# Kernel optimization log

Hardware: AMD Instinct MI355X
Metric: run time of the kernel (lower is better)

## Reference

```python
import jax, jax.numpy as jnp
import numpy as np

N = 50000      # nodes
E = 800000     # edges (before self-loops)
IN = 256       # input_dim
HID = 72       # hidden_dim
HEADS = 4
NEG_SLOPE = 0.2  # PyG GATConv default leaky-relu slope


def setup_inputs() -> dict:
    key = jax.random.key(0)
    ks = jax.random.split(key, 16)
    rn = lambda k, shape: jax.random.normal(k, shape, jnp.float32) * 0.05
    return {
        "x": jax.random.normal(ks[0], (N, IN), jnp.float32),
        "edge_index": jax.random.randint(ks[1], (2, E), 0, N),
        "W_in": rn(ks[2], (IN, HID)), "b_in": jnp.zeros((HID,), jnp.float32),
        "W1": rn(ks[3], (HID, HEADS * HID)),
        "a_src1": rn(ks[4], (HEADS, HID)), "a_dst1": rn(ks[5], (HEADS, HID)),
        "b1": jnp.zeros((HEADS * HID,), jnp.float32),
        "W2": rn(ks[6], (HEADS * HID, HID)),
        "a_src2": rn(ks[7], (1, HID)), "a_dst2": rn(ks[8], (1, HID)),
        "b2": jnp.zeros((HID,), jnp.float32),
        "W3": rn(ks[9], (HID, HID)),
        "a_src3": rn(ks[10], (1, HID)), "a_dst3": rn(ks[11], (1, HID)),
        "b3": jnp.zeros((HID,), jnp.float32),
        "Ws1": rn(ks[12], (HID, 32)), "bs1": jnp.zeros((32,), jnp.float32),
        "Ws2": rn(ks[13], (32, 1)), "bs2": jnp.zeros((1,), jnp.float32),
    }


def gat_conv(x, src, dst, W, a_src, a_dst, bias, concat):
    # PyG GATConv (eval mode): per-head linear, leaky-relu attention logits,
    # segment softmax over incoming edges per destination, scatter-aggregate.
    H, C = a_src.shape
    h = (x @ W).reshape(-1, H, C)                      # [N, H, C]
    logit_s = jnp.einsum('nhc,hc->nh', h, a_src)       # [N, H]
    logit_d = jnp.einsum('nhc,hc->nh', h, a_dst)       # [N, H]
    e = jax.nn.leaky_relu(logit_s[src] + logit_d[dst], NEG_SLOPE)   # [Et, H]
    emax = jax.ops.segment_max(e, dst, num_segments=N)
    emax = jnp.where(jnp.isfinite(emax), emax, 0.0)
    p = jnp.exp(e - emax[dst])
    denom = jax.ops.segment_sum(p, dst, num_segments=N)
    alpha = p / jnp.maximum(denom[dst], 1e-16)         # [Et, H]
    out = jax.ops.segment_sum(h[src] * alpha[:, :, None], dst, num_segments=N)
    out = out.reshape(-1, H * C) if concat else out.mean(axis=1)
    return out + bias


def reference(x, edge_index, W_in, b_in,
              W1, a_src1, a_dst1, b1,
              W2, a_src2, a_dst2, b2,
              W3, a_src3, a_dst3, b3,
              Ws1, bs1, Ws2, bs2):
    loops = jnp.arange(N)                              # PyG add_self_loops=True
    src = jnp.concatenate([edge_index[0], loops])
    dst = jnp.concatenate([edge_index[1], loops])
    x0 = x @ W_in + b_in                               # [N, HID]
    h = jax.nn.elu(gat_conv(x0, src, dst, W1, a_src1, a_dst1, b1, True))
    h = jax.nn.elu(gat_conv(h, src, dst, W2, a_src2, a_dst2, b2, False))
    h = jax.nn.elu(gat_conv(h, src, dst, W3, a_src3, a_dst3, b3, False))
    h = h + x0
    score = jax.nn.relu(h @ Ws1 + bs1) @ Ws2 + bs2     # dropout = identity (eval)
    return score.squeeze(-1)                           # [N]
```

## Files before the change

### kernel.cpp

```cpp
#include <hip/hip_runtime.h>
#include <hip/hip_fp16.h>
#include <cmath>

#define NN 50000
#define EE 800000
#define ET (EE + NN)
#define IN_DIM 256
#define HID 72
#define CAP 96

typedef __attribute__((ext_vector_type(8))) short s8v;
typedef __attribute__((ext_vector_type(4))) short s4v;
typedef __attribute__((ext_vector_type(4))) float f4v;
typedef __attribute__((ext_vector_type(2))) float f2v;

__device__ __forceinline__ ushort f2bf(float x) {
    uint u = __float_as_uint(x);
    return (ushort)((u + 0x7fffu + ((u >> 16) & 1u)) >> 16);
}
__device__ __forceinline__ float bf2f(ushort h) {
    return __uint_as_float(((uint)h) << 16);
}
__device__ __forceinline__ void split4(const float4& v, s4v& h, s4v& l) {
    ushort h0 = f2bf(v.x), h1 = f2bf(v.y), h2 = f2bf(v.z), h3 = f2bf(v.w);
    h = (s4v){(short)h0, (short)h1, (short)h2, (short)h3};
    l = (s4v){(short)f2bf(v.x - bf2f(h0)), (short)f2bf(v.y - bf2f(h1)),
              (short)f2bf(v.z - bf2f(h2)), (short)f2bf(v.w - bf2f(h3))};
}
__device__ __forceinline__ f4v mfma16(s8v a, s8v b, f4v c) {
    return __builtin_amdgcn_mfma_f32_16x16x32_bf16(a, b, c, 0, 0, 0);
}
__device__ __forceinline__ f2v unpack_h2(uint pv) {
    __half2 hv = __builtin_bit_cast(__half2, pv);
    return (f2v){__low2float(hv), __high2float(hv)};
}
__device__ __forceinline__ uint pack_h2(float a, float b) {
    __half2 hp = __floats2half2_rn(a, b);
    return __builtin_bit_cast(uint, hp);
}
__device__ __forceinline__ f2v fma2(float w, f2v c, f2v a) {
    return __builtin_elementwise_fma((f2v){w, w}, c, a);
}

__device__ __forceinline__ void wsplit_one(const float* W, int ldw, int K,
        int idx, short* outH, short* outL) {
    int h = idx / (72 * K);
    int rem = idx - h * 72 * K;
    int n = rem / K, k = rem - n * K;
    float v = W[(size_t)k * ldw + h * 72 + n];
    ushort hi = f2bf(v);
    outH[idx] = (short)hi;
    outL[idx] = (short)f2bf(v - bf2f(hi));
}

#define PR0 18432
#define PR1 (PR0 + 20736)
#define PR2 (PR1 + 20736)
#define PR3 (PR2 + 5184)
#define PR4 (PR3 + 288)
#define PRTOT (PR4 + NN)

__global__ __launch_bounds__(256) void prep_kernel(
        const float* __restrict__ W_in, const float* __restrict__ W1,
        const float* __restrict__ W2, const float* __restrict__ W3,
        const float* __restrict__ a_src, const float* __restrict__ a_dst,
        short* __restrict__ BtInH, short* __restrict__ BtInL,
        short* __restrict__ Bt1H, short* __restrict__ Bt1L,
        short* __restrict__ Bt2H, short* __restrict__ Bt2L,
        short* __restrict__ Bt3H, short* __restrict__ Bt3L,
        float* __restrict__ wsrc, float* __restrict__ wdst,
        int* __restrict__ deg, ushort* __restrict__ ell) {
    int gid = blockIdx.x * 256 + threadIdx.x;
    if (gid < PR0) {
        wsplit_one(W_in, 72, 256, gid, BtInH, BtInL);
    } else if (gid < PR1) {
        wsplit_one(W1, 288, 72, gid - PR0, Bt1H, Bt1L);
    } else if (gid < PR2) {
        wsplit_one(W2, 72, 288, gid - PR1, Bt2H, Bt2L);
    } else if (gid < PR3) {
        wsplit_one(W3, 72, 72, gid - PR2, Bt3H, Bt3L);
    } else if (gid < PR4) {
        int j = gid - PR3;
        int h = j / HID, k = j % HID;
        const float* wrow = W1 + (size_t)k * (4 * HID) + h * HID;
        const float* as = a_src + h * HID;
        const float* ad = a_dst + h * HID;
        float s = 0.f, d = 0.f;
        for (int c = 0; c < HID; ++c) {
            float w = wrow[c];
            s = fmaf(w, as[c], s);
            d = fmaf(w, ad[c], d);
        }
        wsrc[j] = s;
        wdst[j] = d;
    } else if (gid < PRTOT) {
        int i = gid - PR4;
        deg[i] = 1;
        ell[(size_t)i * CAP] = (ushort)i;
    }
}

template <int NLOGIT, bool ELU_EPI, bool BATCHED, bool PACKOUT, bool APACK, bool ADJ>
__global__ __launch_bounds__(256) void gemm_mfma(
        const void* __restrict__ Ain, const short* __restrict__ BtH,
        const short* __restrict__ BtL, const float* __restrict__ bias,
        float* __restrict__ C, uint* __restrict__ Cp, int ldp,
        const float* __restrict__ lvs, const float* __restrict__ lvd,
        float* __restrict__ ls, float* __restrict__ ld,
        int M, int K, int lda, int Nfull,
        const int* __restrict__ eiw, int* __restrict__ degw,
        ushort* __restrict__ ellw, int gemmBlocks) {
    __shared__ __align__(16) short AhS[64 * 40], AlS[64 * 40];
    __shared__ __align__(16) short BhS[80 * 40], BlS[80 * 40];

    int tid = threadIdx.x;

    if (ADJ && (int)blockIdx.x >= gemmBlocks) {
        int t = (blockIdx.x - gemmBlocks) * 256 + tid;
        int i0 = t * 4;
        if (i0 < EE) {
            int4 s4 = *(const int4*)(eiw + i0);
            int4 d4 = *(const int4*)(eiw + EE + i0);
            int ss[4] = {s4.x, s4.y, s4.z, s4.w};
            int dd[4] = {d4.x, d4.y, d4.z, d4.w};
            #pragma unroll
            for (int u = 0; u < 4; ++u) {
                int pos = atomicAdd(&degw[dd[u]], 1);
                if (pos < CAP) ellw[(size_t)dd[u] * CAP + pos] = (ushort)ss[u];
            }
        }
        return;
    }

    int row0 = blockIdx.x * 64;
    int hh = BATCHED ? blockIdx.y : 0;
    int aoff = BATCHED ? hh * (APACK ? 36 : 72) : 0;
    int coff = BATCHED ? hh * 72 : 0;
    const short* bhg = BtH + (size_t)hh * 72 * K;
    const short* blg = BtL + (size_t)hh * 72 * K;

    for (int i = tid; i < 8 * 40; i += 256) {
        BhS[72 * 40 + i] = 0;
        BlS[72 * 40 + i] = 0;
    }

    int w = tid >> 6;
    int lane = tid & 63;
    int q = lane >> 4, l16 = lane & 15;

    f4v acc[5];
    #pragma unroll
    for (int f = 0; f < 5; ++f) acc[f] = (f4v)0.f;

    int ar = tid >> 2;
    int aseg = tid & 3;
    bool arok = (row0 + ar) < M;
    const float* aptrf = nullptr;
    const uint*  aptru = nullptr;
    if constexpr (APACK) {
        aptru = (const uint*)Ain + (size_t)(row0 + ar) * lda + aoff;
    } else {
        aptrf = (const float*)Ain + (size_t)(row0 + ar) * lda + aoff;
    }
    int bn0 = tid >> 2, bq0 = tid & 3;
    int bn1 = (tid + 256) >> 2;

    float4 va, vb;
    s8v bh0, bl0, bh1, bl1;
    auto gload = [&](int k0) {
        va = (float4){0, 0, 0, 0};
        vb = (float4){0, 0, 0, 0};
        int ka = k0 + aseg * 8;
        if constexpr (APACK) {
            if (arok && ka < K) {
                uint4 u = *(const uint4*)(aptru + (ka >> 1));
                f2v p0 = unpack_h2(u.x), p1 = unpack_h2(u.y);
                f2v p2 = unpack_h2(u.z), p3 = unpack_h2(u.w);
                va = (float4){p0.x, p0.y, p1.x, p1.y};
                vb = (float4){p2.x, p2.y, p3.x, p3.y};
            }
        } else {
            if (arok && ka < K)     va = *(const float4*)(aptrf + ka);
            if (arok && ka + 4 < K) vb = *(const float4*)(aptrf + ka + 4);
        }
        bh0 = (s8v)0; bl0 = (s8v)0;
        int kb = k0 + bq0 * 8;
        if (kb < K) {
            bh0 = *(const s8v*)(bhg + (size_t)bn0 * K + kb);
            bl0 = *(const s8v*)(blg + (size_t)bn0 * K + kb);
        }
        bh1 = (s8v)0; bl1 = (s8v)0;
        if (tid < 32 && kb < K) {
            bh1 = *(const s8v*)(bhg + (size_t)bn1 * K + kb);
            bl1 = *(const s8v*)(blg + (size_t)bn1 * K + kb);
        }
    };
    auto commit = [&]() {
        s4v h0, l0, h1, l1;
        split4(va, h0, l0);
        split4(vb, h1, l1);
        *(s4v*)&AhS[ar * 40 + aseg * 8]     = h0;
        *(s4v*)&AhS[ar * 40 + aseg * 8 + 4] = h1;
        *(s4v*)&AlS[ar * 40 + aseg * 8]     = l0;
        *(s4v*)&AlS[ar * 40 + aseg * 8 + 4] = l1;
        *(s8v*)&BhS[bn0 * 40 + bq0 * 8] = bh0;
        *(s8v*)&BlS[bn0 * 40 + bq0 * 8] = bl0;
        if (tid < 32) {
            *(s8v*)&BhS[bn1 * 40 + bq0 * 8] = bh1;
            *(s8v*)&BlS[bn1 * 40 + bq0 * 8] = bl1;
        }
    };

    int ntiles = (K + 31) / 32;
    gload(0);
    for (int t = 0; t < ntiles; ++t) {
        commit();
        __syncthreads();
        if (t + 1 < ntiles) gload((t + 1) * 32);
        s8v ah = *(const s8v*)&AhS[(w * 16 + l16) * 40 + q * 8];
        s8v al = *(const s8v*)&AlS[(w * 16 + l16) * 40 + q * 8];
        #pragma unroll
        for (int f = 0; f < 5; ++f) {
            s8v bh = *(const s8v*)&BhS[(f * 16 + l16) * 40 + q * 8];
            s8v bl = *(const s8v*)&BlS[(f * 16 + l16) * 40 + q * 8];
            acc[f] = mfma16(ah, bh, acc[f]);
            acc[f] = mfma16(ah, bl, acc[f]);
            acc[f] = mfma16(al, bh, acc[f]);
        }
        __syncthreads();
    }

    float v[5][4];
    #pragma unroll
    for (int f = 0; f < 5; ++f) {
        int col = f * 16 + l16;
        bool cv = col < 72;
        #pragma unroll
        for (int r = 0; r < 4; ++r) {
            float t = acc[f][r];
            if (cv && bias) t += bias[coff + col];
            if (ELU_EPI) t = (t > 0.f) ? t : expm1f(t);
            v[f][r] = cv ? t : 0.f;
        }
    }
    if (NLOGIT > 0) {
        #pragma unroll
        for (int h2 = 0; h2 < NLOGIT; ++h2) {
            #pragma unroll
            for (int r = 0; r < 4; ++r) {
                float s = 0.f, d = 0.f;
                #pragma unroll
                for (int f = 0; f < 5; ++f) {
                    int col = f * 16 + l16;
                    float lw = (col < 72) ? lvs[h2 * 72 + col] : 0.f;
                    float dw = (col < 72) ? lvd[h2 * 72 + col] : 0.f;
                    s = fmaf(v[f][r], lw, s);
                    d = fmaf(v[f][r], dw, d);
                }
                s += __shfl_xor(s, 1); s += __shfl_xor(s, 2);
                s += __shfl_xor(s, 4); s += __shfl_xor(s, 8);
                d += __shfl_xor(d, 1); d += __shfl_xor(d, 2);
                d += __shfl_xor(d, 4); d += __shfl_xor(d, 8);
                int gr = row0 + w * 16 + q * 4 + r;
                if (l16 == 0 && gr < M) {
                    ls[gr * NLOGIT + h2] = s;
                    ld[gr * NLOGIT + h2] = d;
                }
            }
        }
    }
    if (PACKOUT) {
        #pragma unroll
        for (int f = 0; f < 5; ++f) {
            int col = f * 16 + l16;
            #pragma unroll
            for (int r = 0; r < 4; ++r) {
                float vo = __shfl_xor(v[f][r], 1);
                if ((l16 & 1) == 0 && col < 72) {
                    int gr = row0 + w * 16 + q * 4 + r;
                    if (gr < M) {
                        Cp[(size_t)gr * ldp + ((coff + col) >> 1)] =
                            pack_h2(v[f][r], vo);
                    }
                }
            }
        }
    }
    if (C != nullptr) {
        #pragma unroll
        for (int f = 0; f < 5; ++f) {
            int col = f * 16 + l16;
            if (col >= 72) continue;
            #pragma unroll
            for (int r = 0; r < 4; ++r) {
                int gr = row0 + w * 16 + q * 4 + r;
                if (gr < M) C[(size_t)gr * Nfull + coff + col] = v[f][r];
            }
        }
    }
}

template <int H, bool EPI, bool ADD_RES, bool POUT, bool SCORE>
__global__ __launch_bounds__(64) void agg_gather(
        const uint* __restrict__ featp,
        const float* __restrict__ ls, const float* __restrict__ ld,
        const int* __restrict__ degv, const ushort* __restrict__ ell,
        const float* __restrict__ bias, const float* __restrict__ res,
        float* __restrict__ out, uint* __restrict__ outp,
        const float* __restrict__ Ws1, const float* __restrict__ bs1,
        const float* __restrict__ Ws2, const float* __restrict__ bs2,
        int n) {
    __shared__ float wsh[64 * H];
    __shared__ int ssh[64];
    __shared__ float srow[HID];
    int wid = blockIdx.x;
    int lane = threadIdx.x;
    int deg = min(degv[wid], CAP);
    const ushort* row = ell + (size_t)wid * CAP;

    float ldh[H];
    if (H == 4) {
        float4 t = ((const float4*)ld)[wid];
        ldh[0] = t.x; ldh[1] = t.y; ldh[2] = t.z; ldh[3] = t.w;
    } else {
        ldh[0] = ld[wid];
    }

    f2v acc2[H];
    #pragma unroll
    for (int h = 0; h < H; ++h) acc2[h] = (f2v)0.f;

    if (deg <= 64) {
        bool act = lane < deg;
        int s = row[act ? lane : 0];
        ssh[lane] = s;
        float e[H];
        float ev[H];
        if (H == 4) {
            float4 lv = ((const float4*)ls)[s];
            ev[0] = lv.x; ev[1] = lv.y; ev[2] = lv.z; ev[3] = lv.w;
        } else {
            ev[0] = ls[s];
        }
        #pragma unroll
        for (int h = 0; h < H; ++h) {
            float vv = ev[h] + ldh[h];
            vv = (vv > 0.f) ? vv : 0.2f * vv;
            e[h] = act ? vv : -__builtin_inff();
        }
        float wv[H];
        #pragma unroll
        for (int h = 0; h < H; ++h) {
            float mh = e[h];
            #pragma unroll
            for (int off = 32; off; off >>= 1) mh = fmaxf(mh, __shfl_xor(mh, off));
            float ph = act ? expf(e[h] - mh) : 0.f;
            float sh = ph;
            #pragma unroll
            for (int off = 32; off; off >>= 1) sh += __shfl_xor(sh, off);
            wv[h] = ph / fmaxf(sh, 1e-16f);
        }
        if (H == 4) {
            ((float4*)wsh)[lane] = (float4){wv[0], wv[1], wv[2], wv[3]};
        } else {
            wsh[lane] = wv[0];
        }
        __syncthreads();

        int nb = (deg + 7) & ~7;
        const uint* rowbase = featp + (lane < 36 ? lane : 0);
        for (int t = 0; t < nb; t += 8) {
            int si[8];
            #pragma unroll
            for (int u = 0; u < 8; ++u) si[u] = ssh[t + u];
            uint pv[8];
            #pragma unroll
            for (int u = 0; u < 8; ++u) pv[u] = rowbase[(size_t)si[u] * 36];
            #pragma unroll
            for (int u = 0; u < 8; ++u) {
                f2v c2 = unpack_h2(pv[u]);
                if constexpr (H == 4) {
                    float4 we = ((const float4*)wsh)[t + u];
                    acc2[0] = fma2(we.x, c2, acc2[0]);
                    acc2[1] = fma2(we.y, c2, acc2[1]);
                    acc2[2] = fma2(we.z, c2, acc2[2]);
                    acc2[3] = fma2(we.w, c2, acc2[3]);
                } else {
                    acc2[0] = fma2(wsh[t + u], c2, acc2[0]);
                }
            }
        }
    } else {
        float m[H];
        #pragma unroll
        for (int h = 0; h < H; ++h) m[h] = -__builtin_inff();
        for (int i = lane; i < deg; i += 64) {
            int s = row[i];
            float e[H];
            if (H == 4) {
                float4 lv = ((const float4*)ls)[s];
                e[0] = lv.x; e[1] = lv.y; e[2] = lv.z; e[3] = lv.w;
            } else {
                e[0] = ls[s];
            }
            #pragma unroll
            for (int h = 0; h < H; ++h) {
                float vv = e[h] + ldh[h];
                vv = (vv > 0.f) ? vv : 0.2f * vv;
                m[h] = fmaxf(m[h], vv);
            }
        }
        #pragma unroll
        for (int h = 0; h < H; ++h)
            #pragma unroll
            for (int off = 32; off; off >>= 1) m[h] = fmaxf(m[h], __shfl_xor(m[h], off));

        float ssum[H];
        #pragma unroll
        for (int h = 0; h < H; ++h) ssum[h] = 0.f;
        for (int i = lane; i < deg; i += 64) {
            int s = row[i];
            float e[H];
            if (H == 4) {
                float4 lv = ((const float4*)ls)[s];
                e[0] = lv.x; e[1] = lv.y; e[2] = lv.z; e[3] = lv.w;
            } else {
                e[0] = ls[s];
            }
            #pragma unroll
            for (int h = 0; h < H; ++h) {
                float vv = e[h] + ldh[h];
                vv = (vv > 0.f) ? vv : 0.2f * vv;
                ssum[h] += expf(vv - m[h]);
            }
        }
        #pragma unroll
        for (int h = 0; h < H; ++h)
            #pragma unroll
            for (int off = 32; off; off >>= 1) ssum[h] += __shfl_xor(ssum[h], off);
        float inv[H];
        #pragma unroll
        for (int h = 0; h < H; ++h) inv[h] = 1.f / fmaxf(ssum[h], 1e-16f);

        for (int base = 0; base < deg; base += 64) {
            int i = base + lane;
            int lim = min(64, deg - base);
            if (i < deg) {
                int s = row[i];
                ssh[lane] = s;
                float e[H];
                if (H == 4) {
                    float4 lv = ((const float4*)ls)[s];
                    e[0] = lv.x; e[1] = lv.y; e[2] = lv.z; e[3] = lv.w;
                } else {
                    e[0] = ls[s];
                }
                if (H == 4) {
                    float p0 = expf(((e[0] + ldh[0] > 0.f) ? e[0] + ldh[0] : 0.2f * (e[0] + ldh[0])) - m[0]) * inv[0];
                    float p1 = expf(((e[1] + ldh[1] > 0.f) ? e[1] + ldh[1] : 0.2f * (e[1] + ldh[1])) - m[1]) * inv[1];
                    float p2 = expf(((e[2] + ldh[2] > 0.f) ? e[2] + ldh[2] : 0.2f * (e[2] + ldh[2])) - m[2]) * inv[2];
                    float p3 = expf(((e[3] + ldh[3] > 0.f) ? e[3] + ldh[3] : 0.2f * (e[3] + ldh[3])) - m[3]) * inv[3];
                    ((float4*)wsh)[lane] = (float4){p0, p1, p2, p3};
                } else {
                    float vv = e[0] + ldh[0];
                    vv = (vv > 0.f) ? vv : 0.2f * vv;
                    wsh[lane] = expf(vv - m[0]) * inv[0];
                }
            }
            __syncthreads();
            for (int t = 0; t < lim; ++t) {
                uint pv = featp[(size_t)ssh[t] * 36 + (lane < 36 ? lane : 0)];
                f2v c2 = unpack_h2(pv);
                if constexpr (H == 4) {
                    float4 we = ((const float4*)wsh)[t];
                    acc2[0] = fma2(we.x, c2, acc2[0]);
                    acc2[1] = fma2(we.y, c2, acc2[1]);
                    acc2[2] = fma2(we.z, c2, acc2[2]);
                    acc2[3] = fma2(we.w, c2, acc2[3]);
                } else {
                    acc2[0] = fma2(wsh[t], c2, acc2[0]);
                }
            }
            __syncthreads();
        }
    }

    if (lane < 36) {
        #pragma unroll
        for (int h = 0; h < H; ++h) {
            float v0 = acc2[h].x, v1 = acc2[h].y;
            if (EPI) {
                v0 += bias[2 * lane];
                v1 += bias[2 * lane + 1];
                v0 = (v0 > 0.f) ? v0 : expm1f(v0);
                v1 = (v1 > 0.f) ? v1 : expm1f(v1);
                if (ADD_RES) {
                    float2 rr = *(const float2*)&res[(size_t)wid * HID + 2 * lane];
                    v0 += rr.x; v1 += rr.y;
                }
            }
            if (POUT) {
                outp[(size_t)wid * (H * 36) + h * 36 + lane] = pack_h2(v0, v1);
            } else if (SCORE) {
                srow[2 * lane] = v0;
                srow[2 * lane + 1] = v1;
            } else {
                *(float2*)&out[(size_t)wid * (H * HID) + h * HID + 2 * lane] =
                    (float2){v0, v1};
            }
        }
    }
    if (SCORE) {
        __syncthreads();
        if (lane < 32) {
            float acc = bs1[lane];
            #pragma unroll 8
            for (int c = 0; c < HID; ++c)
                acc = fmaf(srow[c], Ws1[c * 32 + lane], acc);
            float v = fmaxf(acc, 0.f) * Ws2[lane];
            #pragma unroll
            for (int off = 16; off; off >>= 1) v += __shfl_down(v, off, 32);
            if (lane == 0) out[wid] = v + bs2[0];
        }
    }
}

extern "C" void kernel_launch(void* const* d_in, const int* in_sizes, int n_in,
                              void* d_out, int out_size, void* d_ws, size_t ws_size,
                              hipStream_t stream) {
    const float* x      = (const float*)d_in[0];
    const int*   ei     = (const int*)  d_in[1];
    const float* W_in   = (const float*)d_in[2];
    const float* b_in   = (const float*)d_in[3];
    const float* W1     = (const float*)d_in[4];
    const float* a_src1 = (const float*)d_in[5];
    const float* a_dst1 = (const float*)d_in[6];
    const float* b1     = (const float*)d_in[7];
    const float* W2     = (const float*)d_in[8];
    const float* a_src2 = (const float*)d_in[9];
    const float* a_dst2 = (const float*)d_in[10];
    const float* b2     = (const float*)d_in[11];
    const float* W3     = (const float*)d_in[12];
    const float* a_src3 = (const float*)d_in[13];
    const float* a_dst3 = (const float*)d_in[14];
    const float* b3     = (const float*)d_in[15];
    const float* Ws1    = (const float*)d_in[16];
    const float* bs1    = (const float*)d_in[17];
    const float* Ws2    = (const float*)d_in[18];
    const float* bs2    = (const float*)d_in[19];
    float* out = (float*)d_out;

    float* ws    = (float*)d_ws;
    float* x0    = ws;
    float* ls    = x0 + (size_t)NN * HID;
    float* ld    = ls + (size_t)NN * 4;
    float* wsrc1 = ld + (size_t)NN * 4;
    float* wdst1 = wsrc1 + 288;
    int* deg     = (int*)(wdst1 + 288);
    ushort* ell  = (ushort*)(deg + NN);
    uintptr_t bp = ((uintptr_t)(ell + (size_t)NN * CAP) + 15) & ~(uintptr_t)15;
    short* BtInH = (short*)bp;
    short* BtInL = BtInH + 18432;
    short* Bt1H  = BtInL + 18432;
    short* Bt1L  = Bt1H + 20736;
    short* Bt2H  = Bt1L + 20736;
    short* Bt2L  = Bt2H + 20736;
    short* Bt3H  = Bt2L + 20736;
    short* Bt3L  = Bt3H + 5184;
    uint*  x0p   = (uint*)(Bt3L + 5184);
    uint*  a1p   = x0p + (size_t)NN * 36;
    uint*  h1p   = a1p + (size_t)NN * 144;
    uint*  hp2p  = h1p + (size_t)NN * 144;
    uint*  h2p   = hp2p + (size_t)NN * 36;
    uint*  hp3p  = h2p + (size_t)NN * 36;

    prep_kernel<<<(PRTOT + 255) / 256, 256, 0, stream>>>(
        W_in, W1, W2, W3, a_src1, a_dst1,
        BtInH, BtInL, Bt1H, Bt1L, Bt2H, Bt2L, Bt3H, Bt3L, wsrc1, wdst1,
        deg, ell);

    const int mblocks = (NN + 63) / 64;
    const int adjBlocks = (EE / 4 + 255) / 256;
    gemm_mfma<4, false, false, true, false, true>
        <<<dim3(mblocks + adjBlocks, 1), 256, 0, stream>>>(
        x, BtInH, BtInL, b_in, x0, x0p, 36, wsrc1, wdst1, ls, ld,
        NN, IN_DIM, IN_DIM, HID, ei, deg, ell, mblocks);
    agg_gather<4, false, false, true, false><<<NN, 64, 0, stream>>>(
        x0p, ls, ld, deg, ell, nullptr, nullptr, nullptr, a1p,
        nullptr, nullptr, nullptr, nullptr, NN);
    gemm_mfma<0, true, true, true, true, false><<<dim3(mblocks, 4), 256, 0, stream>>>(
        a1p, Bt1H, Bt1L, b1, nullptr, h1p, 144, nullptr, nullptr, nullptr, nullptr,
        NN, HID, 144, 0, nullptr, nullptr, nullptr, 0);
    gemm_mfma<1, false, false, true, true, false><<<dim3(mblocks, 1), 256, 0, stream>>>(
        h1p, Bt2H, Bt2L, nullptr, nullptr, hp2p, 36, a_src2, a_dst2, ls, ld,
        NN, 288, 144, 0, nullptr, nullptr, nullptr, 0);
    agg_gather<1, true, false, true, false><<<NN, 64, 0, stream>>>(
        hp2p, ls, ld, deg, ell, b2, nullptr, nullptr, h2p,
        nullptr, nullptr, nullptr, nullptr, NN);
    gemm_mfma<1, false, false, true, true, false><<<dim3(mblocks, 1), 256, 0, stream>>>(
        h2p, Bt3H, Bt3L, nullptr, nullptr, hp3p, 36, a_src3, a_dst3, ls, ld,
        NN, HID, 36, 0, nullptr, nullptr, nullptr, 0);
    agg_gather<1, true, true, false, true><<<NN, 64, 0, stream>>>(
        hp3p, ls, ld, deg, ell, b3, x0, out, nullptr,
        Ws1, bs1, Ws2, bs2, NN);
}
```

Measured before the change: 366.2 us.

## Fuse edge aggregation with following per-node GEMM into one agg_gemm kernel

Adds an agg_gemm kernel in which each 256-thread block gathers and softmax-aggregates 64 destination nodes into shared memory as fp16. It then runs the next layer's split-bf16 MFMA GEMM directly from that tile, with optional bias/ELU and attention-logit epilogues. It replaces the layer-1 agg+GEMM pair and the layer-2 agg + layer-3 GEMM pair, removing intermediate a1p/h2p global round-trips and two launches. Layer-3 logits go to separate ls3/ld3 buffers so ls/ld, which are still being read by other blocks, are not overwritten. The trade-off is lower parallelism during the gather phase: each wave now processes 16 nodes serially instead of one node per 64-thread block.

```diff
diff --git a/kernel.cpp b/kernel.cpp
--- a/kernel.cpp
+++ b/kernel.cpp
@@ -40,6 +40,17 @@
 }
 __device__ __forceinline__ f2v fma2(float w, f2v c, f2v a) {
     return __builtin_elementwise_fma((f2v){w, w}, c, a);
+}
+__device__ __forceinline__ void unpack_split8(uint4 u, s8v& ah, s8v& al) {
+    f2v p0 = unpack_h2(u.x), p1 = unpack_h2(u.y);
+    f2v p2 = unpack_h2(u.z), p3 = unpack_h2(u.w);
+    float x[8] = {p0.x, p0.y, p1.x, p1.y, p2.x, p2.y, p3.x, p3.y};
+    #pragma unroll
+    for (int i = 0; i < 8; ++i) {
+        ushort hi = f2bf(x[i]);
+        ah[i] = (short)hi;
+        al[i] = (short)f2bf(x[i] - bf2f(hi));
+    }
 }
 
 __device__ __forceinline__ void wsplit_one(const float* W, int ldw, int K,
@@ -300,6 +311,271 @@
     }
 }
 
+template <int H, int NH, bool AGG_EPI, int NLOGIT, bool GELU>
+__global__ __launch_bounds__(256) void agg_gemm(
+        const uint* __restrict__ featp,
+        const float* __restrict__ ls, const float* __restrict__ ld,
+        const int* __restrict__ degv, const ushort* __restrict__ ell,
+        const float* __restrict__ abias,
+        const short* __restrict__ BtH, const short* __restrict__ BtL,
+        const float* __restrict__ gbias,
+        const float* __restrict__ lvs, const float* __restrict__ lvd,
+        float* __restrict__ lso, float* __restrict__ ldo,
+        uint* __restrict__ outp, int ldp) {
+    __shared__ __align__(16) uint aS[64][H * 36 + 4];
+    int tid = threadIdx.x;
+    int w = tid >> 6;
+    int lane = tid & 63;
+    int row0 = blockIdx.x * 64;
+
+    for (int i = 0; i < 16; ++i) {
+        int nl = w * 16 + i;
+        int n = row0 + nl;
+        if (n >= NN) {
+            if (lane < 36) {
+                #pragma unroll
+                for (int h = 0; h < H; ++h) aS[nl][h * 36 + lane] = 0u;
+            }
+            continue;
+        }
+        int deg = min(degv[n], CAP);
+        const ushort* row = ell + (size_t)n * CAP;
+        float ldh[H];
+        if (H == 4) {
+            float4 t = ((const float4*)ld)[n];
+            ldh[0] = t.x; ldh[1] = t.y; ldh[2] = t.z; ldh[3] = t.w;
+        } else {
+            ldh[0] = ld[n];
+        }
+        f2v acc2[H];
+        #pragma unroll
+        for (int h = 0; h < H; ++h) acc2[h] = (f2v)0.f;
+        const uint* rowbase = featp + (lane < 36 ? lane : 0);
+
+        if (deg <= 64) {
+            bool act = lane < deg;
+            int s = row[act ? lane : 0];
+            float ev[H];
+            if (H == 4) {
+                float4 lv = ((const float4*)ls)[s];
+                ev[0] = lv.x; ev[1] = lv.y; ev[2] = lv.z; ev[3] = lv.w;
+            } else {
+                ev[0] = ls[s];
+            }
+            float wv[H];
+            #pragma unroll
+            for (int h = 0; h < H; ++h) {
+                float vv = ev[h] + ldh[h];
+                vv = (vv > 0.f) ? vv : 0.2f * vv;
+                float e = act ? vv : -__builtin_inff();
+                float mh = e;
+                #pragma unroll
+                for (int off = 32; off; off >>= 1) mh = fmaxf(mh, __shfl_xor(mh, off));
+                float ph = act ? expf(e - mh) : 0.f;
+                float sh = ph;
+                #pragma unroll
+                for (int off = 32; off; off >>= 1) sh += __shfl_xor(sh, off);
+                wv[h] = ph / fmaxf(sh, 1e-16f);
+            }
+            int nb = (deg + 7) & ~7;
+            for (int t = 0; t < nb; t += 8) {
+                int si[8];
+                #pragma unroll
+                for (int u = 0; u < 8; ++u) si[u] = __shfl(s, t + u);
+                uint pv[8];
+                #pragma unroll
+                for (int u = 0; u < 8; ++u) pv[u] = rowbase[(size_t)si[u] * 36];
+                #pragma unroll
+                for (int u = 0; u < 8; ++u) {
+                    f2v c2 = unpack_h2(pv[u]);
+                    #pragma unroll
+                    for (int h = 0; h < H; ++h) {
+                        float wu = __shfl(wv[h], t + u);
+                        acc2[h] = fma2(wu, c2, acc2[h]);
+                    }
+                }
+            }
+        } else {
+            float m[H];
+            #pragma unroll
+            for (int h = 0; h < H; ++h) m[h] = -__builtin_inff();
+            for (int i2 = lane; i2 < deg; i2 += 64) {
+                int s = row[i2];
+                float ev[H];
+                if (H == 4) {
+                    float4 lv = ((const float4*)ls)[s];
+                    ev[0] = lv.x; ev[1] = lv.y; ev[2] = lv.z; ev[3] = lv.w;
+                } else {
+                    ev[0] = ls[s];
+                }
+                #pragma unroll
+                for (int h = 0; h < H; ++h) {
+                    float vv = ev[h] + ldh[h];
+                    vv = (vv > 0.f) ? vv : 0.2f * vv;
+                    m[h] = fmaxf(m[h], vv);
+                }
+            }
+            #pragma unroll
+            for (int h = 0; h < H; ++h)
+                #pragma unroll
+                for (int off = 32; off; off >>= 1) m[h] = fmaxf(m[h], __shfl_xor(m[h], off));
+            float ssum[H];
+            #pragma unroll
+            for (int h = 0; h < H; ++h) ssum[h] = 0.f;
+            for (int i2 = lane; i2 < deg; i2 += 64) {
+                int s = row[i2];
+                float ev[H];
+                if (H == 4) {
+                    float4 lv = ((const float4*)ls)[s];
+                    ev[0] = lv.x; ev[1] = lv.y; ev[2] = lv.z; ev[3] = lv.w;
+                } else {
+                    ev[0] = ls[s];
+                }
+                #pragma unroll
+                for (int h = 0; h < H; ++h) {
+                    float vv = ev[h] + ldh[h];
+                    vv = (vv > 0.f) ? vv : 0.2f * vv;
+                    ssum[h] += expf(vv - m[h]);
+                }
+            }
+            #pragma unroll
+            for (int h = 0; h < H; ++h)
+                #pragma unroll
+                for (int off = 32; off; off >>= 1) ssum[h] += __shfl_xor(ssum[h], off);
+            float inv[H];
+            #pragma unroll
+            for (int h = 0; h < H; ++h) inv[h] = 1.f / fmaxf(ssum[h], 1e-16f);
+            for (int base = 0; base < deg; base += 64) {
+                int i2 = base + lane;
+                int lim = min(64, deg - base);
+                int s = row[(i2 < deg) ? i2 : base];
+                float pw[H];
+                float ev[H];
+                if (H == 4) {
+                    float4 lv = ((const float4*)ls)[s];
+                    ev[0] = lv.x; ev[1] = lv.y; ev[2] = lv.z; ev[3] = lv.w;
+                } else {
+                    ev[0] = ls[s];
+                }
+                #pragma unroll
+                for (int h = 0; h < H; ++h) {
+                    float vv = ev[h] + ldh[h];
+                    vv = (vv > 0.f) ? vv : 0.2f * vv;
+                    pw[h] = (i2 < deg) ? expf(vv - m[h]) * inv[h] : 0.f;
+                }
+                for (int t = 0; t < lim; ++t) {
+                    int sv = __shfl(s, t);
+                    uint pv = rowbase[(size_t)sv * 36];
+                    f2v c2 = unpack_h2(pv);
+                    #pragma unroll
+                    for (int h = 0; h < H; ++h) {
+                        float wu = __shfl(pw[h], t);
+                        acc2[h] = fma2(wu, c2, acc2[h]);
+                    }
+                }
+            }
+        }
+
+        if (lane < 36) {
+            #pragma unroll
+            for (int h = 0; h < H; ++h) {
+                float v0 = acc2[h].x, v1 = acc2[h].y;
+                if (AGG_EPI) {
+                    v0 += abias[2 * lane];
+                    v1 += abias[2 * lane + 1];
+                    v0 = (v0 > 0.f) ? v0 : expm1f(v0);
+                    v1 = (v1 > 0.f) ? v1 : expm1f(v1);
+                }
+                aS[nl][h * 36 + lane] = pack_h2(v0, v1);
+            }
+        }
+    }
+    __syncthreads();
+
+    int q = lane >> 4, l16 = lane & 15;
+    int arow = w * 16 + l16;
+    for (int h = 0; h < NH; ++h) {
+        f4v acc[5];
+        #pragma unroll
+        for (int f = 0; f < 5; ++f) acc[f] = (f4v)0.f;
+        #pragma unroll
+        for (int t3 = 0; t3 < 3; ++t3) {
+            int ks = t3 * 32 + q * 8;
+            s8v ah = (s8v)0, al = (s8v)0;
+            if (ks < 72) {
+                uint4 u = *(const uint4*)&aS[arow][h * 36 + (ks >> 1)];
+                unpack_split8(u, ah, al);
+            }
+            #pragma unroll
+            for (int f = 0; f < 5; ++f) {
+                int bn = f * 16 + l16;
+                s8v bh = (s8v)0, bl = (s8v)0;
+                if (bn < 72 && ks < 72) {
+                    bh = *(const s8v*)(BtH + ((size_t)h * 72 + bn) * 72 + ks);
+                    bl = *(const s8v*)(BtL + ((size_t)h * 72 + bn) * 72 + ks);
+                }
+                acc[f] = mfma16(ah, bh, acc[f]);
+                acc[f] = mfma16(ah, bl, acc[f]);
+                acc[f] = mfma16(al, bh, acc[f]);
+            }
+        }
+        float v[5][4];
+        #pragma unroll
+        for (int f = 0; f < 5; ++f) {
+            int col = f * 16 + l16;
+            bool cv = col < 72;
+            #pragma unroll
+            for (int r = 0; r < 4; ++r) {
+                float t = acc[f][r];
+                if (cv && gbias) t += gbias[h * 72 + col];
+                if (GELU) t = (t > 0.f) ? t : expm1f(t);
+                v[f][r] = cv ? t : 0.f;
+            }
+        }
+        if (NLOGIT > 0) {
+            #pragma unroll
+            for (int h2 = 0; h2 < NLOGIT; ++h2) {
+                #pragma unroll
+                for (int r = 0; r < 4; ++r) {
+                    float s = 0.f, d = 0.f;
+                    #pragma unroll
+                    for (int f = 0; f < 5; ++f) {
+                        int col = f * 16 + l16;
+                        float lw = (col < 72) ? lvs[h2 * 72 + col] : 0.f;
+                        float dw = (col < 72) ? lvd[h2 * 72 + col] : 0.f;
+                        s = fmaf(v[f][r], lw, s);
+                        d = fmaf(v[f][r], dw, d);
+                    }
+                    s += __shfl_xor(s, 1); s += __shfl_xor(s, 2);
+                    s += __shfl_xor(s, 4); s += __shfl_xor(s, 8);
+                    d += __shfl_xor(d, 1); d += __shfl_xor(d, 2);
+                    d += __shfl_xor(d, 4); d += __shfl_xor(d, 8);
+                    int gr = row0 + w * 16 + q * 4 + r;
+                    if (l16 == 0 && gr < NN) {
+                        lso[gr * NLOGIT + h2] = s;
+                        ldo[gr * NLOGIT + h2] = d;
+                    }
+                }
+            }
+        }
+        #pragma unroll
+        for (int f = 0; f < 5; ++f) {
+            int col = f * 16 + l16;
+            #pragma unroll
+            for (int r = 0; r < 4; ++r) {
+                float vo = __shfl_xor(v[f][r], 1);
+                if ((l16 & 1) == 0 && col < 72) {
+                    int gr = row0 + w * 16 + q * 4 + r;
+                    if (gr < NN) {
+                        outp[(size_t)gr * ldp + h * 36 + (col >> 1)] =
+                            pack_h2(v[f][r], vo);
+                    }
+                }
+            }
+        }
+    }
+}
+
 template <int H, bool EPI, bool ADD_RES, bool POUT, bool SCORE>
 __global__ __launch_bounds__(64) void agg_gather(
         const uint* __restrict__ featp,
@@ -554,7 +830,9 @@
     float* x0    = ws;
     float* ls    = x0 + (size_t)NN * HID;
     float* ld    = ls + (size_t)NN * 4;
-    float* wsrc1 = ld + (size_t)NN * 4;
+    float* ls3   = ld + (size_t)NN * 4;
+    float* ld3   = ls3 + NN;
+    float* wsrc1 = ld3 + NN;
     float* wdst1 = wsrc1 + 288;
     int* deg     = (int*)(wdst1 + 288);
     ushort* ell  = (ushort*)(deg + NN);
@@ -568,11 +846,9 @@
     short* Bt3H  = Bt2L + 20736;
     short* Bt3L  = Bt3H + 5184;
     uint*  x0p   = (uint*)(Bt3L + 5184);
-    uint*  a1p   = x0p + (size_t)NN * 36;
-    uint*  h1p   = a1p + (size_t)NN * 144;
+    uint*  h1p   = x0p + (size_t)NN * 36;
     uint*  hp2p  = h1p + (size_t)NN * 144;
-    uint*  h2p   = hp2p + (size_t)NN * 36;
-    uint*  hp3p  = h2p + (size_t)NN * 36;
+    uint*  hp3p  = hp2p + (size_t)NN * 36;
 
     prep_kernel<<<(PRTOT + 255) / 256, 256, 0, stream>>>(
         W_in, W1, W2, W3, a_src1, a_dst1,
@@ -585,22 +861,16 @@
         <<<dim3(mblocks + adjBlocks, 1), 256, 0, stream>>>(
         x, BtInH, BtInL, b_in, x0, x0p, 36, wsrc1, wdst1, ls, ld,
         NN, IN_DIM, IN_DIM, HID, ei, deg, ell, mblocks);
-    agg_gather<4, false, false, true, false><<<NN, 64, 0, stream>>>(
-        x0p, ls, ld, deg, ell, nullptr, nullptr, nullptr, a1p,
-        nullptr, nullptr, nullptr, nullptr, NN);
-    gemm_mfma<0, true, true, true, true, false><<<dim3(mblocks, 4), 256, 0, stream>>>(
-        a1p, Bt1H, Bt1L, b1, nullptr, h1p, 144, nullptr, nullptr, nullptr, nullptr,
-        NN, HID, 144, 0, nullptr, nullptr, nullptr, 0);
+    agg_gemm<4, 4, false, 0, true><<<mblocks, 256, 0, stream>>>(
+        x0p, ls, ld, deg, ell, nullptr, Bt1H, Bt1L, b1,
+        nullptr, nullptr, nullptr, nullptr, h1p, 144);
     gemm_mfma<1, false, false, true, true, false><<<dim3(mblocks, 1), 256, 0, stream>>>(
         h1p, Bt2H, Bt2L, nullptr, nullptr, hp2p, 36, a_src2, a_dst2, ls, ld,
         NN, 288, 144, 0, nullptr, nullptr, nullptr, 0);
-    agg_gather<1, true, false, true, false><<<NN, 64, 0, stream>>>(
-        hp2p, ls, ld, deg, ell, b2, nullptr, nullptr, h2p,
-        nullptr, nullptr, nullptr, nullptr, NN);
-    gemm_mfma<1, false, false, true, true, false><<<dim3(mblocks, 1), 256, 0, stream>>>(
-        h2p, Bt3H, Bt3L, nullptr, nullptr, hp3p, 36, a_src3, a_dst3, ls, ld,
-        NN, HID, 36, 0, nullptr, nullptr, nullptr, 0);
+    agg_gemm<1, 1, true, 1, false><<<mblocks, 256, 0, stream>>>(
+        hp2p, ls, ld, deg, ell, b2, Bt3H, Bt3L, nullptr,
+        a_src3, a_dst3, ls3, ld3, hp3p, 36);
     agg_gather<1, true, true, false, true><<<NN, 64, 0, stream>>>(
-        hp3p, ls, ld, deg, ell, b3, x0, out, nullptr,
+        hp3p, ls3, ld3, deg, ell, b3, x0, out, nullptr,
         Ws1, bs1, Ws2, bs2, NN);
 }
```

After: 484.5 us. 1.32x slower.

## Fuse layer-1 per-head GEMM and layer-2 GEMM into one kernel via shared memory

Applied to the files above, without the earlier changes.

Adds a gemm12 kernel that computes the layer-1 per-head transform with bias and ELU, keeps the 64x288 result as packed fp16 in shared memory, then runs the layer-2 GEMM and attention-logit reductions from it. This removes the h1p intermediate (N x 288 fp16) round trip to global memory and one kernel launch. Layer-3 logits now go to separate ls3/ld3 buffers, presumably because ls/ld are still read by the layer-2 aggregation. In exchange each block does all four heads serially, so the grid is a quarter the size of the old 4-way grid, and a large shared array may reduce occupancy.

```diff
diff --git a/kernel.cpp b/kernel.cpp
--- a/kernel.cpp
+++ b/kernel.cpp
@@ -40,6 +40,17 @@
 }
 __device__ __forceinline__ f2v fma2(float w, f2v c, f2v a) {
     return __builtin_elementwise_fma((f2v){w, w}, c, a);
+}
+__device__ __forceinline__ void unpack_split8(uint4 u, s8v& ah, s8v& al) {
+    f2v p0 = unpack_h2(u.x), p1 = unpack_h2(u.y);
+    f2v p2 = unpack_h2(u.z), p3 = unpack_h2(u.w);
+    float x[8] = {p0.x, p0.y, p1.x, p1.y, p2.x, p2.y, p3.x, p3.y};
+    #pragma unroll
+    for (int i = 0; i < 8; ++i) {
+        ushort hi = f2bf(x[i]);
+        ah[i] = (short)hi;
+        al[i] = (short)f2bf(x[i] - bf2f(hi));
+    }
 }
 
 __device__ __forceinline__ void wsplit_one(const float* W, int ldw, int K,
@@ -300,6 +311,136 @@
     }
 }
 
+__global__ __launch_bounds__(256) void gemm12(
+        const uint* __restrict__ a1p,
+        const short* __restrict__ B1H, const short* __restrict__ B1L,
+        const float* __restrict__ b1,
+        const short* __restrict__ B2H, const short* __restrict__ B2L,
+        const float* __restrict__ lvs, const float* __restrict__ lvd,
+        float* __restrict__ lso, float* __restrict__ ldo,
+        uint* __restrict__ outp) {
+    __shared__ __align__(16) uint hS[64][148];
+    int tid = threadIdx.x;
+    int w = tid >> 6;
+    int lane = tid & 63;
+    int q = lane >> 4, l16 = lane & 15;
+    int row0 = blockIdx.x * 64;
+    int arow = w * 16 + l16;
+    int gra = row0 + arow;
+    bool aok = gra < NN;
+    const uint* abase = a1p + (size_t)(aok ? gra : 0) * 144;
+
+    #pragma unroll
+    for (int h = 0; h < 4; ++h) {
+        f4v acc[5];
+        #pragma unroll
+        for (int f = 0; f < 5; ++f) acc[f] = (f4v)0.f;
+        #pragma unroll
+        for (int t3 = 0; t3 < 3; ++t3) {
+            int ks = t3 * 32 + q * 8;
+            s8v ah = (s8v)0, al = (s8v)0;
+            if (aok && ks < 72) {
+                uint4 u = *(const uint4*)(abase + h * 36 + (ks >> 1));
+                unpack_split8(u, ah, al);
+            }
+            #pragma unroll
+            for (int f = 0; f < 5; ++f) {
+                int bn = f * 16 + l16;
+                s8v bh = (s8v)0, bl = (s8v)0;
+                if (bn < 72 && ks < 72) {
+                    bh = *(const s8v*)(B1H + ((size_t)h * 72 + bn) * 72 + ks);
+                    bl = *(const s8v*)(B1L + ((size_t)h * 72 + bn) * 72 + ks);
+                }
+                acc[f] = mfma16(ah, bh, acc[f]);
+                acc[f] = mfma16(ah, bl, acc[f]);
+                acc[f] = mfma16(al, bh, acc[f]);
+            }
+        }
+        #pragma unroll
+        for (int f = 0; f < 5; ++f) {
+            int col = f * 16 + l16;
+            bool cv = col < 72;
+            #pragma unroll
+            for (int r = 0; r < 4; ++r) {
+                float t = acc[f][r];
+                if (cv) {
+                    t += b1[h * 72 + col];
+                    t = (t > 0.f) ? t : expm1f(t);
+                }
+                float ve = cv ? t : 0.f;
+                float vo = __shfl_xor(ve, 1);
+                if ((l16 & 1) == 0 && col < 72) {
+                    hS[w * 16 + q * 4 + r][h * 36 + (col >> 1)] = pack_h2(ve, vo);
+                }
+            }
+        }
+    }
+
+    f4v acc[5];
+    #pragma unroll
+    for (int f = 0; f < 5; ++f) acc[f] = (f4v)0.f;
+    #pragma unroll
+    for (int t = 0; t < 9; ++t) {
+        int ks = t * 32 + q * 8;
+        uint4 u = *(const uint4*)&hS[arow][ks >> 1];
+        s8v ah, al;
+        unpack_split8(u, ah, al);
+        #pragma unroll
+        for (int f = 0; f < 5; ++f) {
+            int bn = f * 16 + l16;
+            s8v bh = (s8v)0, bl = (s8v)0;
+            if (bn < 72) {
+                bh = *(const s8v*)(B2H + (size_t)bn * 288 + ks);
+                bl = *(const s8v*)(B2L + (size_t)bn * 288 + ks);
+            }
+            acc[f] = mfma16(ah, bh, acc[f]);
+            acc[f] = mfma16(ah, bl, acc[f]);
+            acc[f] = mfma16(al, bh, acc[f]);
+        }
+    }
+    float v[5][4];
+    #pragma unroll
+    for (int f = 0; f < 5; ++f) {
+        int col = f * 16 + l16;
+        bool cv = col < 72;
+        #pragma unroll
+        for (int r = 0; r < 4; ++r) v[f][r] = cv ? acc[f][r] : 0.f;
+    }
+    #pragma unroll
+    for (int r = 0; r < 4; ++r) {
+        float s = 0.f, d = 0.f;
+        #pragma unroll
+        for (int f = 0; f < 5; ++f) {
+            int col = f * 16 + l16;
+            float lw = (col < 72) ? lvs[col] : 0.f;
+            float dw = (col < 72) ? lvd[col] : 0.f;
+            s = fmaf(v[f][r], lw, s);
+            d = fmaf(v[f][r], dw, d);
+        }
+        s += __shfl_xor(s, 1); s += __shfl_xor(s, 2);
+        s += __shfl_xor(s, 4); s += __shfl_xor(s, 8);
+        d += __shfl_xor(d, 1); d += __shfl_xor(d, 2);
+        d += __shfl_xor(d, 4); d += __shfl_xor(d, 8);
+        int gr = row0 + w * 16 + q * 4 + r;
+        if (l16 == 0 && gr < NN) {
+            lso[gr] = s;
+            ldo[gr] = d;
+        }
+    }
+    #pragma unroll
+    for (int f = 0; f < 5; ++f) {
+        int col = f * 16 + l16;
+        #pragma unroll
+        for (int r = 0; r < 4; ++r) {
+            float vo = __shfl_xor(v[f][r], 1);
+            if ((l16 & 1) == 0 && col < 72) {
+                int gr = row0 + w * 16 + q * 4 + r;
+                if (gr < NN) outp[(size_t)gr * 36 + (col >> 1)] = pack_h2(v[f][r], vo);
+            }
+        }
+    }
+}
+
 template <int H, bool EPI, bool ADD_RES, bool POUT, bool SCORE>
 __global__ __launch_bounds__(64) void agg_gather(
         const uint* __restrict__ featp,
@@ -554,7 +695,9 @@
     float* x0    = ws;
     float* ls    = x0 + (size_t)NN * HID;
     float* ld    = ls + (size_t)NN * 4;
-    float* wsrc1 = ld + (size_t)NN * 4;
+    float* ls3   = ld + (size_t)NN * 4;
+    float* ld3   = ls3 + NN;
+    float* wsrc1 = ld3 + NN;
     float* wdst1 = wsrc1 + 288;
     int* deg     = (int*)(wdst1 + 288);
     ushort* ell  = (ushort*)(deg + NN);
@@ -569,8 +712,7 @@
     short* Bt3L  = Bt3H + 5184;
     uint*  x0p   = (uint*)(Bt3L + 5184);
     uint*  a1p   = x0p + (size_t)NN * 36;
-    uint*  h1p   = a1p + (size_t)NN * 144;
-    uint*  hp2p  = h1p + (size_t)NN * 144;
+    uint*  hp2p  = a1p + (size_t)NN * 144;
     uint*  h2p   = hp2p + (size_t)NN * 36;
     uint*  hp3p  = h2p + (size_t)NN * 36;
 
@@ -588,19 +730,15 @@
     agg_gather<4, false, false, true, false><<<NN, 64, 0, stream>>>(
         x0p, ls, ld, deg, ell, nullptr, nullptr, nullptr, a1p,
         nullptr, nullptr, nullptr, nullptr, NN);
-    gemm_mfma<0, true, true, true, true, false><<<dim3(mblocks, 4), 256, 0, stream>>>(
-        a1p, Bt1H, Bt1L, b1, nullptr, h1p, 144, nullptr, nullptr, nullptr, nullptr,
-        NN, HID, 144, 0, nullptr, nullptr, nullptr, 0);
-    gemm_mfma<1, false, false, true, true, false><<<dim3(mblocks, 1), 256, 0, stream>>>(
-        h1p, Bt2H, Bt2L, nullptr, nullptr, hp2p, 36, a_src2, a_dst2, ls, ld,
-        NN, 288, 144, 0, nullptr, nullptr, nullptr, 0);
+    gemm12<<<mblocks, 256, 0, stream>>>(
+        a1p, Bt1H, Bt1L, b1, Bt2H, Bt2L, a_src2, a_dst2, ls, ld, hp2p);
     agg_gather<1, true, false, true, false><<<NN, 64, 0, stream>>>(
         hp2p, ls, ld, deg, ell, b2, nullptr, nullptr, h2p,
         nullptr, nullptr, nullptr, nullptr, NN);
     gemm_mfma<1, false, false, true, true, false><<<dim3(mblocks, 1), 256, 0, stream>>>(
-        h2p, Bt3H, Bt3L, nullptr, nullptr, hp3p, 36, a_src3, a_dst3, ls, ld,
+        h2p, Bt3H, Bt3L, nullptr, nullptr, hp3p, 36, a_src3, a_dst3, ls3, ld3,
         NN, HID, 36, 0, nullptr, nullptr, nullptr, 0);
     agg_gather<1, true, true, false, true><<<NN, 64, 0, stream>>>(
-        hp3p, ls, ld, deg, ell, b3, x0, out, nullptr,
+        hp3p, ls3, ld3, deg, ell, b3, x0, out, nullptr,
         Ws1, bs1, Ws2, bs2, NN);
 }
```

New measurement: 368.4 us. Within noise of the previous version (+0.6%).
